# Kernel tuning notes

Measured on AMD Instinct MI355X. Metric: run time of the kernel, lower is better.

The kernel has to match this reference:

```python
import jax, jax.numpy as jnp
import numpy as np

N_NODES = 100000
N_EDGES = 1200000
D_IN = 16
D_EDGE = 4
H = 64


def setup_inputs() -> dict:
    key = jax.random.key(0)
    ks = jax.random.split(key, 20)
    s = 0.05
    inp = {
        "src": jax.random.randint(ks[0], (N_EDGES,), 0, N_NODES),
        "dst": jax.random.randint(ks[1], (N_EDGES,), 0, N_NODES),
        "t": jax.random.uniform(ks[2], (N_EDGES,), dtype=jnp.float32),
        "x": jax.random.normal(ks[3], (N_NODES, D_IN), dtype=jnp.float32),
        "edge_attr": jax.random.normal(ks[4], (N_EDGES, D_EDGE), dtype=jnp.float32),
        # x_encoder
        "Wx": jax.random.normal(ks[5], (D_IN, H), dtype=jnp.float32) * s,
        "bx": jnp.zeros((H,), dtype=jnp.float32),
        # TransformerConv (heads=1, concat=False)
        "Wq": jax.random.normal(ks[6], (H, H), dtype=jnp.float32) * s,
        "bq": jnp.zeros((H,), dtype=jnp.float32),
        "Wk": jax.random.normal(ks[7], (H, H), dtype=jnp.float32) * s,
        "bk": jnp.zeros((H,), dtype=jnp.float32),
        "Wv": jax.random.normal(ks[8], (H, H), dtype=jnp.float32) * s,
        "bv": jnp.zeros((H,), dtype=jnp.float32),
        "We": jax.random.normal(ks[9], (D_EDGE, H), dtype=jnp.float32) * s,  # lin_edge, bias=False
        "Ws": jax.random.normal(ks[10], (H, H), dtype=jnp.float32) * s,  # lin_skip (root weight)
        "bs": jnp.zeros((H,), dtype=jnp.float32),
        # MLP head
        "W1": jax.random.normal(ks[11], (H, 8), dtype=jnp.float32) * s,
        "b1": jnp.zeros((8,), dtype=jnp.float32),
        "W2": jax.random.normal(ks[12], (8, 1), dtype=jnp.float32) * s,
        "b2": jnp.zeros((1,), dtype=jnp.float32),
    }
    return inp


def reference(src, dst, t, x, edge_attr, Wx, bx, Wq, bq, Wk, bk, Wv, bv, We, Ws, bs, W1, b1, W2, b2):
    # eval mode: dropouts are identity; TGN memory.update_state is a pure
    # side effect and does not influence the returned output.
    xe = x @ Wx + bx                             # [N, H]

    # TransformerConv, heads=1, concat=False, flow src -> dst
    q = xe @ Wq + bq                             # [N, H]
    k = xe @ Wk + bk                             # [N, H]
    v = xe @ Wv + bv                             # [N, H]
    e = edge_attr @ We                           # [E, H]

    k_e = k[src] + e                             # [E, H]
    v_e = v[src] + e                             # [E, H]
    alpha = jnp.sum(q[dst] * k_e, axis=-1) / jnp.sqrt(jnp.float32(H))  # [E]

    # softmax over incoming edges per destination node
    m = jax.ops.segment_max(alpha, dst, num_segments=N_NODES)
    a = jnp.exp(alpha - m[dst])
    denom = jax.ops.segment_sum(a, dst, num_segments=N_NODES)
    w = a / (denom[dst] + 1e-16)                 # [E]

    agg = jax.ops.segment_sum(v_e * w[:, None], dst, num_segments=N_NODES)  # [N, H]
    h_local = agg + (xe @ Ws + bs)               # root/skip connection

    h = h_local[dst]                             # [E, H]
    h = jax.nn.relu(h @ W1 + b1)                 # [E, 8]
    out = (h @ W2 + b2)[:, 0]                    # [E]
    return out
```

## Files before the change

kernel.cpp:

```cpp
#include <hip/hip_runtime.h>

#define OFF_M   0
#define OFF_U   256
#define OFF_W   272
#define OFF_C   288
#define OFF_R   292
#define OFF_R0  356
#define OFF_PV  360
#define OFF_PE  488
#define OFF_PS  520
#define OFF_BH1 648
#define OFF_BH2 656
#define CST_N   664

struct Params {
    const int* src; const int* dst; const float4* ea4; const float* x;
    const float* Wx; const float* bx;
    const float* Wq; const float* bq;
    const float* Wk; const float* bk;
    const float* Wv; const float* bv;
    const float* We; const float* Ws; const float* bs;
    const float* W1; const float* b1; const float* W2; const float* b2;
    float* cst;
    float* yv;
    float* pv;
    float* xps;
    float* H;
    float4* rv4;
    float* den;
    float* g;
    float* out;
    int N, E;
};

__device__ void do_fold(const Params& P, float* __restrict__ cst)
{
    __shared__ float sWf[4][16][64];
    __shared__ float sbf[4][64];
    const int t = threadIdx.x;
    const int c = t & 63, m = t >> 6;
    const float* W; const float* b;
    switch (m) {
        case 0:  W = P.Wq; b = P.bq; break;
        case 1:  W = P.Wk; b = P.bk; break;
        case 2:  W = P.Wv; b = P.bv; break;
        default: W = P.Ws; b = P.bs; break;
    }
    float acc[16];
#pragma unroll
    for (int i = 0; i < 16; ++i) acc[i] = 0.f;
    float bacc = b[c];
    for (int j = 0; j < 64; ++j) {
        const float wv = W[j * 64 + c];
        bacc += P.bx[j] * wv;
#pragma unroll
        for (int i = 0; i < 16; ++i) acc[i] += P.Wx[i * 64 + j] * wv;
    }
#pragma unroll
    for (int i = 0; i < 16; ++i) sWf[m][i][c] = acc[i];
    sbf[m][c] = bacc;
    __syncthreads();

    {
        const int i = t >> 4, j = t & 15;
        float s = 0.f;
        for (int cc = 0; cc < 64; ++cc) s += sWf[0][i][cc] * sWf[1][j][cc];
        cst[OFF_M + i * 16 + j] = s;
    }
    if (t < 16) {
        float su = 0.f, sw = 0.f;
        for (int cc = 0; cc < 64; ++cc) {
            su += sWf[1][t][cc] * sbf[0][cc];
            sw += sWf[0][t][cc] * sbf[1][cc];
        }
        cst[OFF_U + t] = su;
        cst[OFF_W + t] = sw;
    }
    if (t == 0) {
        float s = 0.f;
        for (int cc = 0; cc < 64; ++cc) s += sbf[0][cc] * sbf[1][cc];
        cst[OFF_C] = s;
    }
    if (t < 64) {
        const int j = t >> 4, i = t & 15;
        float s = 0.f;
        for (int cc = 0; cc < 64; ++cc) s += P.We[j * 64 + cc] * sWf[0][i][cc];
        cst[OFF_R + j * 16 + i] = s;
    }
    if (t < 4) {
        float s = 0.f;
        for (int cc = 0; cc < 64; ++cc) s += P.We[t * 64 + cc] * sbf[0][cc];
        cst[OFF_R0 + t] = s;
    }
    if (t < 128) {
        const int i = t >> 3, j = t & 7;
        float sv = 0.f, ss = 0.f;
        for (int cc = 0; cc < 64; ++cc) {
            const float w1 = P.W1[cc * 8 + j];
            sv += sWf[2][i][cc] * w1;
            ss += sWf[3][i][cc] * w1;
        }
        cst[OFF_PV + i * 8 + j] = sv;
        cst[OFF_PS + i * 8 + j] = ss;
    }
    if (t < 32) {
        const int mm = t >> 3, j = t & 7;
        float s = 0.f;
        for (int cc = 0; cc < 64; ++cc) s += P.We[mm * 64 + cc] * P.W1[cc * 8 + j];
        cst[OFF_PE + mm * 8 + j] = s;
    }
    if (t < 8) {
        float s1 = 0.f, s2 = 0.f;
        for (int cc = 0; cc < 64; ++cc) {
            const float w1 = P.W1[cc * 8 + t];
            s1 += sbf[2][cc] * w1;
            s2 += sbf[3][cc] * w1;
        }
        cst[OFF_BH1 + t] = s1;
        cst[OFF_BH2 + t] = s2 + P.b1[t];
    }
}

__global__ __launch_bounds__(256) void k_init(Params P)
{
    do_fold(P, P.cst);
}

__global__ __launch_bounds__(256) void k_node(Params P)
{
    __shared__ float sx[16][16];
    const float* __restrict__ cst = P.cst;
    const int t = threadIdx.x;
    const int node0 = blockIdx.x * 16;
    const int nl = t >> 4, cg = t & 15;
    {
        const int idx = node0 * 16 + t;
        sx[nl][cg] = (idx < P.N * 16) ? P.x[idx] : 0.f;
    }
    __syncthreads();
    const int n = node0 + nl;
    if (n >= P.N) return;

    float y = cst[OFF_U + cg];
#pragma unroll
    for (int i = 0; i < 16; ++i)
        y += sx[nl][i] * cst[OFF_M + i * 16 + cg];
    P.yv[(size_t)n * 16 + cg] = y;

    if (cg < 8) {
        float s = 0.f;
#pragma unroll
        for (int i = 0; i < 16; ++i)
            s += sx[nl][i] * cst[OFF_PV + i * 8 + cg];
        P.pv[(size_t)n * 8 + cg] = s;
        P.H[(size_t)n * 8 + cg] = 0.f;
    } else {
        const int j = cg - 8;
        float s = 0.f;
#pragma unroll
        for (int i = 0; i < 16; ++i)
            s += sx[nl][i] * cst[OFF_PS + i * 8 + j];
        P.xps[(size_t)n * 8 + j] = s;
    }
    if (cg < 4) {
        float r = cst[OFF_R0 + cg];
#pragma unroll
        for (int i = 0; i < 16; ++i)
            r += cst[OFF_R + cg * 16 + i] * sx[nl][i];
        ((float*)P.rv4)[(size_t)n * 4 + cg] = r;
    } else if (cg == 4) {
        P.den[n] = 0.f;
    }
}

__global__ __launch_bounds__(256) void k_edge(Params P)
{
    const int t = threadIdx.x;
    const int grp = t >> 3;
    const int cg  = t & 7;
    const int e = blockIdx.x * 32 + grp;
    const bool ve = e < P.E;
    const int ee = ve ? e : 0;

    const int s = P.src[ee];
    const int d = P.dst[ee];
    const float4 A = P.ea4[ee];
    const float2 xs2 = ((const float2*)P.x)[(size_t)s * 8 + cg];
    const float2 yd2 = ((const float2*)P.yv)[(size_t)d * 8 + cg];
    const float4 rv = P.rv4[d];

    float p = xs2.x * yd2.x + xs2.y * yd2.y;
    p += __shfl_xor(p, 1);
    p += __shfl_xor(p, 2);
    p += __shfl_xor(p, 4);
    p += A.x * rv.x + A.y * rv.y + A.z * rv.z + A.w * rv.w;
    const float a = __expf(p * 0.125f);

    if (ve) {
        const float* __restrict__ cst = P.cst;
        const float pe = A.x * cst[OFF_PE + 0 * 8 + cg]
                       + A.y * cst[OFF_PE + 1 * 8 + cg]
                       + A.z * cst[OFF_PE + 2 * 8 + cg]
                       + A.w * cst[OFF_PE + 3 * 8 + cg];
        const float pvs = P.pv[(size_t)s * 8 + cg];
        atomicAdd(&P.H[(size_t)d * 8 + cg], a * (pvs + pe));
        if (cg == 0) atomicAdd(&P.den[d], a);
    }
}

__global__ __launch_bounds__(256) void k_fin(Params P)
{
    const int n = blockIdx.x * 256 + threadIdx.x;
    if (n >= P.N) return;
    const float* __restrict__ cst = P.cst;
    const float den = P.den[n];
    const float inv = 1.f / (den + 1e-16f);
    const float dinv = den * inv;
    float val = P.b2[0];
#pragma unroll
    for (int j = 0; j < 8; ++j) {
        const float hid = inv * P.H[(size_t)n * 8 + j]
                        + P.xps[(size_t)n * 8 + j]
                        + dinv * cst[OFF_BH1 + j] + cst[OFF_BH2 + j];
        val += fmaxf(hid, 0.f) * P.W2[j];
    }
    P.g[n] = val;
}

__global__ __launch_bounds__(256) void k_out(
    const int* __restrict__ dst, const float* __restrict__ g,
    float* __restrict__ out, int E)
{
    const int e = blockIdx.x * 256 + threadIdx.x;
    if (e < E) out[e] = g[dst[e]];
}

extern "C" void kernel_launch(void* const* d_in, const int* in_sizes, int n_in,
                              void* d_out, int out_size, void* d_ws, size_t ws_size,
                              hipStream_t stream)
{
    Params P;
    P.src = (const int*)d_in[0];
    P.dst = (const int*)d_in[1];
    P.x   = (const float*)d_in[3];
    P.ea4 = (const float4*)d_in[4];
    P.Wx  = (const float*)d_in[5];
    P.bx  = (const float*)d_in[6];
    P.Wq  = (const float*)d_in[7];
    P.bq  = (const float*)d_in[8];
    P.Wk  = (const float*)d_in[9];
    P.bk  = (const float*)d_in[10];
    P.Wv  = (const float*)d_in[11];
    P.bv  = (const float*)d_in[12];
    P.We  = (const float*)d_in[13];
    P.Ws  = (const float*)d_in[14];
    P.bs  = (const float*)d_in[15];
    P.W1  = (const float*)d_in[16];
    P.b1  = (const float*)d_in[17];
    P.W2  = (const float*)d_in[18];
    P.b2  = (const float*)d_in[19];

    P.E = in_sizes[0];
    P.N = in_sizes[3] / 16;
    P.out = (float*)d_out;

    float* w = (float*)d_ws;
    P.yv  = w;            w += (size_t)P.N * 16;
    P.pv  = w;            w += (size_t)P.N * 8;
    P.xps = w;            w += (size_t)P.N * 8;
    P.H   = w;            w += (size_t)P.N * 8;
    P.rv4 = (float4*)w;   w += (size_t)P.N * 4;
    P.den = w;            w += (size_t)P.N;
    P.g   = w;            w += (size_t)P.N;
    P.cst = w;

    const int nbE = (P.E + 255) / 256;

    k_init<<<1, 256, 0, stream>>>(P);
    k_node<<<(P.N + 15) / 16, 256, 0, stream>>>(P);
    k_edge<<<(P.E + 31) / 32, 256, 0, stream>>>(P);
    k_fin<<<(P.N + 255) / 256, 256, 0, stream>>>(P);
    k_out<<<nbE, 256, 0, stream>>>(P.dst, P.g, P.out, P.E);
}
```

Measured before the change: 283.1 us.

## Pack per-node gather data into 64-byte bf16 records for edge kernel

Per-node source data (x in bf16 plus pv) and destination data (y in bf16 plus rv) are packed into 64-byte records, and the H and den accumulators are merged into one 64-byte record. Each edge then touches one cache line for the source, one for the destination and one for the accumulator, where it used to touch several scattered arrays. The bf16 storage halves the bytes read for the attention dot product. The cost is reduced precision in the attention logits and a larger accumulator footprint.

```diff
diff --git a/kernel.cpp b/kernel.cpp
--- a/kernel.cpp
+++ b/kernel.cpp
@@ -13,6 +13,14 @@
 #define OFF_BH2 656
 #define CST_N   664
 
+__device__ __forceinline__ unsigned f2bf(float f) {
+    unsigned u = __float_as_uint(f);
+    u += 0x7fffu + ((u >> 16) & 1u);
+    return u >> 16;
+}
+__device__ __forceinline__ float bf_lo(unsigned u) { return __uint_as_float(u << 16); }
+__device__ __forceinline__ float bf_hi(unsigned u) { return __uint_as_float(u & 0xffff0000u); }
+
 struct Params {
     const int* src; const int* dst; const float4* ea4; const float* x;
     const float* Wx; const float* bx;
@@ -22,12 +30,10 @@
     const float* We; const float* Ws; const float* bs;
     const float* W1; const float* b1; const float* W2; const float* b2;
     float* cst;
-    float* yv;
-    float* pv;
+    float* srec;
+    float* drec;
+    float* acc;
     float* xps;
-    float* H;
-    float4* rv4;
-    float* den;
     float* g;
     float* out;
     int N, E;
@@ -145,15 +151,21 @@
 #pragma unroll
     for (int i = 0; i < 16; ++i)
         y += sx[nl][i] * cst[OFF_M + i * 16 + cg];
-    P.yv[(size_t)n * 16 + cg] = y;
+
+    const float xv = sx[nl][cg];
+    const float yp = __shfl_xor(y, 1);
+    const float xp = __shfl_xor(xv, 1);
+    if ((cg & 1) == 0) {
+        ((unsigned*)P.drec)[(size_t)n * 16 + (cg >> 1)] = f2bf(y) | (f2bf(yp) << 16);
+        ((unsigned*)P.srec)[(size_t)n * 16 + (cg >> 1)] = f2bf(xv) | (f2bf(xp) << 16);
+    }
 
     if (cg < 8) {
         float s = 0.f;
 #pragma unroll
         for (int i = 0; i < 16; ++i)
             s += sx[nl][i] * cst[OFF_PV + i * 8 + cg];
-        P.pv[(size_t)n * 8 + cg] = s;
-        P.H[(size_t)n * 8 + cg] = 0.f;
+        P.srec[(size_t)n * 16 + 8 + cg] = s;
     } else {
         const int j = cg - 8;
         float s = 0.f;
@@ -167,10 +179,9 @@
 #pragma unroll
         for (int i = 0; i < 16; ++i)
             r += cst[OFF_R + cg * 16 + i] * sx[nl][i];
-        ((float*)P.rv4)[(size_t)n * 4 + cg] = r;
-    } else if (cg == 4) {
-        P.den[n] = 0.f;
-    }
+        P.drec[(size_t)n * 16 + 8 + cg] = r;
+    }
+    P.acc[(size_t)n * 16 + cg] = 0.f;
 }
 
 __global__ __launch_bounds__(256) void k_edge(Params P)
@@ -185,11 +196,12 @@
     const int s = P.src[ee];
     const int d = P.dst[ee];
     const float4 A = P.ea4[ee];
-    const float2 xs2 = ((const float2*)P.x)[(size_t)s * 8 + cg];
-    const float2 yd2 = ((const float2*)P.yv)[(size_t)d * 8 + cg];
-    const float4 rv = P.rv4[d];
-
-    float p = xs2.x * yd2.x + xs2.y * yd2.y;
+    const unsigned xw = ((const unsigned*)P.srec)[(size_t)s * 16 + cg];
+    const float pvs   = P.srec[(size_t)s * 16 + 8 + cg];
+    const unsigned yw = ((const unsigned*)P.drec)[(size_t)d * 16 + cg];
+    const float4 rv   = *(const float4*)&P.drec[(size_t)d * 16 + 8];
+
+    float p = bf_lo(xw) * bf_lo(yw) + bf_hi(xw) * bf_hi(yw);
     p += __shfl_xor(p, 1);
     p += __shfl_xor(p, 2);
     p += __shfl_xor(p, 4);
@@ -202,9 +214,8 @@
                        + A.y * cst[OFF_PE + 1 * 8 + cg]
                        + A.z * cst[OFF_PE + 2 * 8 + cg]
                        + A.w * cst[OFF_PE + 3 * 8 + cg];
-        const float pvs = P.pv[(size_t)s * 8 + cg];
-        atomicAdd(&P.H[(size_t)d * 8 + cg], a * (pvs + pe));
-        if (cg == 0) atomicAdd(&P.den[d], a);
+        atomicAdd(&P.acc[(size_t)d * 16 + cg], a * (pvs + pe));
+        if (cg == 0) atomicAdd(&P.acc[(size_t)d * 16 + 8], a);
     }
 }
 
@@ -213,13 +224,14 @@
     const int n = blockIdx.x * 256 + threadIdx.x;
     if (n >= P.N) return;
     const float* __restrict__ cst = P.cst;
-    const float den = P.den[n];
+    const float* accn = &P.acc[(size_t)n * 16];
+    const float den = accn[8];
     const float inv = 1.f / (den + 1e-16f);
     const float dinv = den * inv;
     float val = P.b2[0];
 #pragma unroll
     for (int j = 0; j < 8; ++j) {
-        const float hid = inv * P.H[(size_t)n * 8 + j]
+        const float hid = inv * accn[j]
                         + P.xps[(size_t)n * 8 + j]
                         + dinv * cst[OFF_BH1 + j] + cst[OFF_BH2 + j];
         val += fmaxf(hid, 0.f) * P.W2[j];
@@ -265,14 +277,12 @@
     P.out = (float*)d_out;
 
     float* w = (float*)d_ws;
-    P.yv  = w;            w += (size_t)P.N * 16;
-    P.pv  = w;            w += (size_t)P.N * 8;
-    P.xps = w;            w += (size_t)P.N * 8;
-    P.H   = w;            w += (size_t)P.N * 8;
-    P.rv4 = (float4*)w;   w += (size_t)P.N * 4;
-    P.den = w;            w += (size_t)P.N;
-    P.g   = w;            w += (size_t)P.N;
-    P.cst = w;
+    P.srec = w;           w += (size_t)P.N * 16;
+    P.drec = w;           w += (size_t)P.N * 16;
+    P.acc  = w;           w += (size_t)P.N * 16;
+    P.xps  = w;           w += (size_t)P.N * 8;
+    P.g    = w;           w += (size_t)P.N;
+    P.cst  = w;
 
     const int nbE = (P.E + 255) / 256;
 
```

Measured after the change: 275.3 us. 2.7% less time.
